# Performance work log

Measured on AMD Instinct MI355X. Metric: run time of the kernel, lower is better.

The kernel has to match this reference:

```python
import jax, jax.numpy as jnp
import numpy as np

B, H, S, D = 4, 16, 2048, 64
INV_SCALE_FACTOR = 8.0  # scores are divided by this (== sqrt(D))
DROPOUT_P = 0.0         # deterministic baseline; dropout is identity at p=0


def setup_inputs() -> dict:
    key = jax.random.key(0)
    kq, kk, kv = jax.random.split(key, 3)
    return {
        "query": jax.random.normal(kq, (B, H, S, D), dtype=jnp.float32),
        "key": jax.random.normal(kk, (B, H, S, D), dtype=jnp.float32),
        "value": jax.random.normal(kv, (B, H, S, D), dtype=jnp.float32),
    }


def reference(query, key, value):
    # scores: [B, H, Sq, Sk]
    scores = jnp.einsum("bhqd,bhkd->bhqk", query, key) / INV_SCALE_FACTOR
    probs = jax.nn.softmax(scores, axis=-1)
    # dropout_p == 0.0 -> identity
    out = jnp.einsum("bhqk,bhkd->bhqd", probs, value)
    return out
```

## Files before the change

kernel.cpp:

```cpp
#include <hip/hip_runtime.h>


#define S_LEN 2048
#define D_DIM 64
#define TK    64
#define NTILE (S_LEN / TK)
#define LOG2E_OVER8 0.18033688011112042f
#define VROW  72
#define VTILE (64 * VROW)
#define VBH   (NTILE * VTILE)

typedef __bf16 bf16x8 __attribute__((ext_vector_type(8)));
typedef __bf16 bf16x4 __attribute__((ext_vector_type(4)));
typedef short  s16x4  __attribute__((ext_vector_type(4)));
typedef float  f32x4  __attribute__((ext_vector_type(4)));
typedef unsigned short us;

__device__ __forceinline__ us f2bf(float f) {
    union { __bf16 h; us u; } c;
    c.h = (__bf16)f;
    return c.u;
}

__device__ __forceinline__ unsigned pk2(float a, float b) {
#if __has_builtin(__builtin_amdgcn_cvt_pk_bf16_f32)
    typedef __bf16 bf2 __attribute__((ext_vector_type(2)));
    union { bf2 h; unsigned u; } c;
    c.h = __builtin_amdgcn_cvt_pk_bf16_f32(a, b);
    return c.u;
#else
    return ((unsigned)f2bf(b) << 16) | f2bf(a);
#endif
}

__device__ __forceinline__ float fast_exp2(float x) {
#if __has_builtin(__builtin_amdgcn_exp2f)
    return __builtin_amdgcn_exp2f(x);
#else
    return exp2f(x);
#endif
}

__device__ __forceinline__ void gload_lds16(const void* g, void* l) {
    __builtin_amdgcn_global_load_lds(
        (const __attribute__((address_space(1))) unsigned int*)g,
        (__attribute__((address_space(3))) unsigned int*)l, 16, 0, 0);
}

__device__ __forceinline__ f32x4 mfma16x16x16(s16x4 a, s16x4 b, f32x4 c) {
#if __has_builtin(__builtin_amdgcn_mfma_f32_16x16x16bf16_1k)
    return __builtin_amdgcn_mfma_f32_16x16x16bf16_1k(a, b, c, 0, 0, 0);
#else
    f32x4 d = c;
    asm volatile("v_mfma_f32_16x16x16_bf16 %0, %1, %2, %0"
                 : "+v"(d) : "v"(a), "v"(b));
    return d;
#endif
}

__global__ __launch_bounds__(256)
void prep(const float* __restrict__ K, const float* __restrict__ V,
          us* __restrict__ Kb, us* __restrict__ Vt) {
    __shared__ us Ls[64 * 68];
    const int bx = blockIdx.x, tid = threadIdx.x;
    if (bx < 4096) {
        const size_t i = ((size_t)bx * 256 + tid) * 8;
        const float4 a = *(const float4*)(K + i);
        const float4 b = *(const float4*)(K + i + 4);
        union { us u[8]; uint4 q; } pk;
        pk.u[0] = f2bf(a.x); pk.u[1] = f2bf(a.y);
        pk.u[2] = f2bf(a.z); pk.u[3] = f2bf(a.w);
        pk.u[4] = f2bf(b.x); pk.u[5] = f2bf(b.y);
        pk.u[6] = f2bf(b.z); pk.u[7] = f2bf(b.w);
        *(uint4*)(Kb + i) = pk.q;
    } else {
        const int idx = bx - 4096;
        const int t = idx & (NTILE - 1), bh = idx >> 5;
        {
            const int r = tid >> 2, seg = tid & 3;
            const float* src = V + ((size_t)bh * S_LEN + t * TK + r) * D_DIM + seg * 16;
            us* dst = &Ls[r * 68 + seg * 16];
#pragma unroll
            for (int i = 0; i < 2; ++i) {
                const float4 v0 = *(const float4*)(src + 8 * i);
                const float4 v1 = *(const float4*)(src + 8 * i + 4);
                union { us u[8]; uint2 q[2]; } pk;
                pk.u[0] = f2bf(v0.x); pk.u[1] = f2bf(v0.y);
                pk.u[2] = f2bf(v0.z); pk.u[3] = f2bf(v0.w);
                pk.u[4] = f2bf(v1.x); pk.u[5] = f2bf(v1.y);
                pk.u[6] = f2bf(v1.z); pk.u[7] = f2bf(v1.w);
                *(uint2*)(dst + 8 * i) = pk.q[0];
                *(uint2*)(dst + 8 * i + 4) = pk.q[1];
            }
        }
        __syncthreads();
        {
            const int d = tid >> 2, sc = tid & 3;
            union { us u[16]; uint4 q[2]; } pk;
#pragma unroll
            for (int j = 0; j < 16; ++j) pk.u[j] = Ls[(sc * 16 + j) * 68 + d];
            us* dst = Vt + (size_t)bh * VBH + t * VTILE + d * VROW + sc * 16;
            *(uint4*)(dst) = pk.q[0];
            *(uint4*)(dst + 8) = pk.q[1];
        }
    }
}

__global__ __launch_bounds__(256, 4)
void fa_fwd(const float* __restrict__ Qg, const us* __restrict__ Kb,
            const us* __restrict__ Vtb, float* __restrict__ Og) {
    __shared__ __align__(16) us Kl[2][TK * 64];
    __shared__ __align__(16) us Vl[2][VTILE];

    const int tid  = threadIdx.x;
    const int w    = tid >> 6;
    const int lane = tid & 63;
    const int l15  = lane & 15;
    const int quad = lane >> 4;
    const int x    = l15 & 7;

    const int bid   = blockIdx.x;
    const int chunk = bid >> 3;
    const int bh    = ((bid & 7) << 3) | (chunk >> 4);
    const int qb    = chunk & 15;
    const size_t base = (size_t)bh * S_LEN * D_DIM;

    bf16x8 bq00, bq01, bq10, bq11;
    {
        const float* q0 = Qg + base + (size_t)(qb * 128 + w * 32 + l15) * D_DIM + quad * 8;
        const float* q1 = q0 + 16 * D_DIM;
#define LOADQ(dst0, dst1, p)                                                  \
        {                                                                     \
            const float4 x0 = *(const float4*)(p);                            \
            const float4 x1 = *(const float4*)((p) + 4);                      \
            const float4 y0 = *(const float4*)((p) + 32);                     \
            const float4 y1 = *(const float4*)((p) + 36);                     \
            dst0[0]=(__bf16)(x0.x*LOG2E_OVER8); dst0[1]=(__bf16)(x0.y*LOG2E_OVER8); \
            dst0[2]=(__bf16)(x0.z*LOG2E_OVER8); dst0[3]=(__bf16)(x0.w*LOG2E_OVER8); \
            dst0[4]=(__bf16)(x1.x*LOG2E_OVER8); dst0[5]=(__bf16)(x1.y*LOG2E_OVER8); \
            dst0[6]=(__bf16)(x1.z*LOG2E_OVER8); dst0[7]=(__bf16)(x1.w*LOG2E_OVER8); \
            dst1[0]=(__bf16)(y0.x*LOG2E_OVER8); dst1[1]=(__bf16)(y0.y*LOG2E_OVER8); \
            dst1[2]=(__bf16)(y0.z*LOG2E_OVER8); dst1[3]=(__bf16)(y0.w*LOG2E_OVER8); \
            dst1[4]=(__bf16)(y1.x*LOG2E_OVER8); dst1[5]=(__bf16)(y1.y*LOG2E_OVER8); \
            dst1[6]=(__bf16)(y1.z*LOG2E_OVER8); dst1[7]=(__bf16)(y1.w*LOG2E_OVER8); \
        }
        LOADQ(bq00, bq01, q0)
        LOADQ(bq10, bq11, q1)
#undef LOADQ
    }

    const int krow   = w * 16 + (lane >> 3);
    const int kchunk = (lane & 7) ^ (lane >> 3);
    const us* ksrc = Kb + base + (size_t)krow * D_DIM + kchunk * 8;
    const us* vsrc = Vtb + (size_t)bh * VBH + lane * 8;

    f32x4 lv0 = {0.f, 0.f, 0.f, 0.f}, lv1 = {0.f, 0.f, 0.f, 0.f};
    f32x4 oa0[4], oa1[4];
#pragma unroll
    for (int db = 0; db < 4; ++db) {
        oa0[db] = (f32x4){0.f, 0.f, 0.f, 0.f};
        oa1[db] = (f32x4){0.f, 0.f, 0.f, 0.f};
    }

#pragma unroll
    for (int j = 0; j < 2; ++j)
        gload_lds16(ksrc + j * 512, &Kl[0][w * 1024 + j * 512]);
#pragma unroll
    for (int j = 0; j < 2; ++j)
        gload_lds16(vsrc + (w * 2 + j) * 512, &Vl[0][(w * 2 + j) * 512]);
    if (w == 0) gload_lds16(vsrc + 8 * 512, &Vl[0][8 * 512]);
    __syncthreads();

#pragma unroll 1
    for (int t = 0; t < NTILE; ++t) {
        const int cur = t & 1;
        if (t + 1 < NTILE) {
            const us* ks = ksrc + (size_t)(t + 1) * (TK * D_DIM);
            const us* vs = vsrc + (size_t)(t + 1) * VTILE;
            us* kd = &Kl[cur ^ 1][w * 1024];
            us* vd = &Vl[cur ^ 1][0];
#pragma unroll
            for (int j = 0; j < 2; ++j)
                gload_lds16(ks + j * 512, kd + j * 512);
#pragma unroll
            for (int j = 0; j < 2; ++j)
                gload_lds16(vs + (w * 2 + j) * 512, vd + (w * 2 + j) * 512);
            if (w == 0) gload_lds16(vs + 8 * 512, vd + 8 * 512);
        }

        const us* kl = Kl[cur];
        const us* vl = Vl[cur];
#pragma unroll
        for (int kb = 0; kb < 4; ++kb) {
            const int row = kb * 16 + l15;
            const bf16x8 a0 = *(const bf16x8*)&kl[row * 64 + ((quad ^ x) * 8)];
            const bf16x8 a1 = *(const bf16x8*)&kl[row * 64 + (((4 + quad) ^ x) * 8)];
            f32x4 c0 = {0.f, 0.f, 0.f, 0.f};
            c0 = __builtin_amdgcn_mfma_f32_16x16x32_bf16(a0, bq00, c0, 0, 0, 0);
            c0 = __builtin_amdgcn_mfma_f32_16x16x32_bf16(a1, bq01, c0, 0, 0, 0);
            f32x4 c1 = {0.f, 0.f, 0.f, 0.f};
            c1 = __builtin_amdgcn_mfma_f32_16x16x32_bf16(a0, bq10, c1, 0, 0, 0);
            c1 = __builtin_amdgcn_mfma_f32_16x16x32_bf16(a1, bq11, c1, 0, 0, 0);

            const float p00 = fast_exp2(c0[0]);
            const float p01 = fast_exp2(c0[1]);
            const float p02 = fast_exp2(c0[2]);
            const float p03 = fast_exp2(c0[3]);
            lv0 += (f32x4){p00, p01, p02, p03};
            const float p10 = fast_exp2(c1[0]);
            const float p11 = fast_exp2(c1[1]);
            const float p12 = fast_exp2(c1[2]);
            const float p13 = fast_exp2(c1[3]);
            lv1 += (f32x4){p10, p11, p12, p13};
            union { unsigned u[2]; s16x4 s; } bu0, bu1;
            bu0.u[0] = pk2(p00, p01);
            bu0.u[1] = pk2(p02, p03);
            bu1.u[0] = pk2(p10, p11);
            bu1.u[1] = pk2(p12, p13);

#pragma unroll
            for (int db = 0; db < 4; ++db) {
                union { bf16x4 h; s16x4 s; } au;
                au.h = *(const bf16x4*)&vl[l15 * VROW + quad * 4 + db * (16 * VROW) + kb * 16];
                oa0[db] = mfma16x16x16(au.s, bu0.s, oa0[db]);
                oa1[db] = mfma16x16x16(au.s, bu1.s, oa1[db]);
            }
        }
        __syncthreads();
    }

    float lq0 = lv0[0] + lv0[1] + lv0[2] + lv0[3];
    lq0 += __shfl_xor(lq0, 16, 64);
    lq0 += __shfl_xor(lq0, 32, 64);
    float lq1 = lv1[0] + lv1[1] + lv1[2] + lv1[3];
    lq1 += __shfl_xor(lq1, 16, 64);
    lq1 += __shfl_xor(lq1, 32, 64);
    const float inv0 = 1.f / lq0;
    const float inv1 = 1.f / lq1;
    float* op0 = Og + base + (size_t)(qb * 128 + w * 32 + l15) * D_DIM + quad * 4;
    float* op1 = op0 + 16 * D_DIM;
#pragma unroll
    for (int db = 0; db < 4; ++db) {
        float4 v0 = { oa0[db][0] * inv0, oa0[db][1] * inv0,
                      oa0[db][2] * inv0, oa0[db][3] * inv0 };
        *(float4*)(op0 + db * 16) = v0;
        float4 v1 = { oa1[db][0] * inv1, oa1[db][1] * inv1,
                      oa1[db][2] * inv1, oa1[db][3] * inv1 };
        *(float4*)(op1 + db * 16) = v1;
    }
}

extern "C" void kernel_launch(void* const* d_in, const int* in_sizes, int n_in,
                              void* d_out, int out_size, void* d_ws, size_t ws_size,
                              hipStream_t stream) {
    const float* Q = (const float*)d_in[0];
    const float* K = (const float*)d_in[1];
    const float* V = (const float*)d_in[2];
    float* O = (float*)d_out;

    us* Kb = (us*)d_ws;
    us* Vt = Kb + (size_t)64 * S_LEN * D_DIM;

    prep<<<4096 + 2048, 256, 0, stream>>>(K, V, Kb, Vt);
    fa_fwd<<<dim3(1024), 256, 0, stream>>>(Q, Kb, Vt, O);
}
```

Before: 235.1 us.

## Load V tiles directly from global into registers in MFMA fragment layout

The preprocessing kernel now writes transposed V in the exact per-lane MFMA A-fragment order, so each lane can fetch its V operands with 16-byte global loads straight into registers. This removes the LDS staging buffer for V and its shared-memory reads, which frees LDS and may raise occupancy. The QK and PV stages are regrouped into pairs of k-blocks so the V global loads can be issued ahead of use. In exchange, V reads now go through global/L2 latency inside the loop with no LDS double buffering, which could stall if the latency is not hidden.

```diff
diff --git a/kernel.cpp b/kernel.cpp
--- a/kernel.cpp
+++ b/kernel.cpp
@@ -6,12 +6,10 @@
 #define TK    64
 #define NTILE (S_LEN / TK)
 #define LOG2E_OVER8 0.18033688011112042f
-#define VROW  72
-#define VTILE (64 * VROW)
+#define VTILE (64 * 64)
 #define VBH   (NTILE * VTILE)
 
 typedef __bf16 bf16x8 __attribute__((ext_vector_type(8)));
-typedef __bf16 bf16x4 __attribute__((ext_vector_type(4)));
 typedef short  s16x4  __attribute__((ext_vector_type(4)));
 typedef float  f32x4  __attribute__((ext_vector_type(4)));
 typedef unsigned short us;
@@ -95,13 +93,20 @@
         }
         __syncthreads();
         {
-            const int d = tid >> 2, sc = tid & 3;
-            union { us u[16]; uint4 q[2]; } pk;
-#pragma unroll
-            for (int j = 0; j < 16; ++j) pk.u[j] = Ls[(sc * 16 + j) * 68 + d];
-            us* dst = Vt + (size_t)bh * VBH + t * VTILE + d * VROW + sc * 16;
-            *(uint4*)(dst) = pk.q[0];
-            *(uint4*)(dst + 8) = pk.q[1];
+            const int lane = tid & 63, db = tid >> 6;
+            const int quad = lane >> 4, l15 = lane & 15;
+            const int d = db * 16 + l15;
+            us* dst = Vt + (size_t)bh * VBH + t * VTILE + lane * 8;
+#pragma unroll
+            for (int c = 0; c < 2; ++c) {
+                union { us u[8]; uint4 q; } pk;
+#pragma unroll
+                for (int e = 0; e < 8; ++e) {
+                    const int k = (2 * c + (e >> 2)) * 16 + quad * 4 + (e & 3);
+                    pk.u[e] = Ls[k * 68 + d];
+                }
+                *(uint4*)(dst + (c * 4 + db) * 512) = pk.q;
+            }
         }
     }
 }
@@ -110,7 +115,6 @@
 void fa_fwd(const float* __restrict__ Qg, const us* __restrict__ Kb,
             const us* __restrict__ Vtb, float* __restrict__ Og) {
     __shared__ __align__(16) us Kl[2][TK * 64];
-    __shared__ __align__(16) us Vl[2][VTILE];
 
     const int tid  = threadIdx.x;
     const int w    = tid >> 6;
@@ -152,9 +156,9 @@
     const int krow   = w * 16 + (lane >> 3);
     const int kchunk = (lane & 7) ^ (lane >> 3);
     const us* ksrc = Kb + base + (size_t)krow * D_DIM + kchunk * 8;
-    const us* vsrc = Vtb + (size_t)bh * VBH + lane * 8;
-
-    f32x4 lv0 = {0.f, 0.f, 0.f, 0.f}, lv1 = {0.f, 0.f, 0.f, 0.f};
+    const us* vg0 = Vtb + (size_t)bh * VBH + lane * 8;
+
+    float lv0 = 0.f, lv1 = 0.f;
     f32x4 oa0[4], oa1[4];
 #pragma unroll
     for (int db = 0; db < 4; ++db) {
@@ -165,74 +169,82 @@
 #pragma unroll
     for (int j = 0; j < 2; ++j)
         gload_lds16(ksrc + j * 512, &Kl[0][w * 1024 + j * 512]);
-#pragma unroll
-    for (int j = 0; j < 2; ++j)
-        gload_lds16(vsrc + (w * 2 + j) * 512, &Vl[0][(w * 2 + j) * 512]);
-    if (w == 0) gload_lds16(vsrc + 8 * 512, &Vl[0][8 * 512]);
     __syncthreads();
+
+    s16x4 bus0[4], bus1[4];
+
+#define QK_STEP(kb)                                                            \
+    {                                                                          \
+        const int row_ = (kb) * 16 + l15;                                      \
+        const bf16x8 a0 = *(const bf16x8*)&kl[row_ * 64 + ((quad ^ x) * 8)];   \
+        const bf16x8 a1 = *(const bf16x8*)&kl[row_ * 64 + (((4 + quad) ^ x) * 8)]; \
+        f32x4 c0 = {0.f, 0.f, 0.f, 0.f};                                       \
+        c0 = __builtin_amdgcn_mfma_f32_16x16x32_bf16(a0, bq00, c0, 0, 0, 0);   \
+        c0 = __builtin_amdgcn_mfma_f32_16x16x32_bf16(a1, bq01, c0, 0, 0, 0);   \
+        f32x4 c1 = {0.f, 0.f, 0.f, 0.f};                                       \
+        c1 = __builtin_amdgcn_mfma_f32_16x16x32_bf16(a0, bq10, c1, 0, 0, 0);   \
+        c1 = __builtin_amdgcn_mfma_f32_16x16x32_bf16(a1, bq11, c1, 0, 0, 0);   \
+        const float p00 = fast_exp2(c0[0]), p01 = fast_exp2(c0[1]);            \
+        const float p02 = fast_exp2(c0[2]), p03 = fast_exp2(c0[3]);            \
+        lv0 += (p00 + p01) + (p02 + p03);                                      \
+        const float p10 = fast_exp2(c1[0]), p11 = fast_exp2(c1[1]);            \
+        const float p12 = fast_exp2(c1[2]), p13 = fast_exp2(c1[3]);            \
+        lv1 += (p10 + p11) + (p12 + p13);                                      \
+        union { unsigned u[2]; s16x4 s; } b0_, b1_;                            \
+        b0_.u[0] = pk2(p00, p01); b0_.u[1] = pk2(p02, p03);                    \
+        b1_.u[0] = pk2(p10, p11); b1_.u[1] = pk2(p12, p13);                    \
+        bus0[kb] = b0_.s; bus1[kb] = b1_.s;                                    \
+    }
+
+#define PV_PAIR(K0)                                                            \
+    _Pragma("unroll")                                                          \
+    for (int db = 0; db < 4; ++db) {                                           \
+        union { uint4 q; s16x4 s[2]; } va;                                     \
+        va.q = vqa[db];                                                        \
+        oa0[db] = mfma16x16x16(va.s[0], bus0[K0], oa0[db]);                    \
+        oa1[db] = mfma16x16x16(va.s[0], bus1[K0], oa1[db]);                    \
+        oa0[db] = mfma16x16x16(va.s[1], bus0[(K0) + 1], oa0[db]);              \
+        oa1[db] = mfma16x16x16(va.s[1], bus1[(K0) + 1], oa1[db]);              \
+    }
 
 #pragma unroll 1
     for (int t = 0; t < NTILE; ++t) {
         const int cur = t & 1;
+        const us* kl = Kl[cur];
+        const us* vg = vg0 + (size_t)t * VTILE;
+
+        uint4 vqa[4];
+#pragma unroll
+        for (int f = 0; f < 4; ++f) vqa[f] = *(const uint4*)(vg + f * 512);
+
+        QK_STEP(0)
+        QK_STEP(1)
+        PV_PAIR(0)
+
+#pragma unroll
+        for (int f = 0; f < 4; ++f) vqa[f] = *(const uint4*)(vg + (4 + f) * 512);
+
         if (t + 1 < NTILE) {
             const us* ks = ksrc + (size_t)(t + 1) * (TK * D_DIM);
-            const us* vs = vsrc + (size_t)(t + 1) * VTILE;
             us* kd = &Kl[cur ^ 1][w * 1024];
-            us* vd = &Vl[cur ^ 1][0];
 #pragma unroll
             for (int j = 0; j < 2; ++j)
                 gload_lds16(ks + j * 512, kd + j * 512);
-#pragma unroll
-            for (int j = 0; j < 2; ++j)
-                gload_lds16(vs + (w * 2 + j) * 512, vd + (w * 2 + j) * 512);
-            if (w == 0) gload_lds16(vs + 8 * 512, vd + 8 * 512);
-        }
-
-        const us* kl = Kl[cur];
-        const us* vl = Vl[cur];
-#pragma unroll
-        for (int kb = 0; kb < 4; ++kb) {
-            const int row = kb * 16 + l15;
-            const bf16x8 a0 = *(const bf16x8*)&kl[row * 64 + ((quad ^ x) * 8)];
-            const bf16x8 a1 = *(const bf16x8*)&kl[row * 64 + (((4 + quad) ^ x) * 8)];
-            f32x4 c0 = {0.f, 0.f, 0.f, 0.f};
-            c0 = __builtin_amdgcn_mfma_f32_16x16x32_bf16(a0, bq00, c0, 0, 0, 0);
-            c0 = __builtin_amdgcn_mfma_f32_16x16x32_bf16(a1, bq01, c0, 0, 0, 0);
-            f32x4 c1 = {0.f, 0.f, 0.f, 0.f};
-            c1 = __builtin_amdgcn_mfma_f32_16x16x32_bf16(a0, bq10, c1, 0, 0, 0);
-            c1 = __builtin_amdgcn_mfma_f32_16x16x32_bf16(a1, bq11, c1, 0, 0, 0);
-
-            const float p00 = fast_exp2(c0[0]);
-            const float p01 = fast_exp2(c0[1]);
-            const float p02 = fast_exp2(c0[2]);
-            const float p03 = fast_exp2(c0[3]);
-            lv0 += (f32x4){p00, p01, p02, p03};
-            const float p10 = fast_exp2(c1[0]);
-            const float p11 = fast_exp2(c1[1]);
-            const float p12 = fast_exp2(c1[2]);
-            const float p13 = fast_exp2(c1[3]);
-            lv1 += (f32x4){p10, p11, p12, p13};
-            union { unsigned u[2]; s16x4 s; } bu0, bu1;
-            bu0.u[0] = pk2(p00, p01);
-            bu0.u[1] = pk2(p02, p03);
-            bu1.u[0] = pk2(p10, p11);
-            bu1.u[1] = pk2(p12, p13);
-
-#pragma unroll
-            for (int db = 0; db < 4; ++db) {
-                union { bf16x4 h; s16x4 s; } au;
-                au.h = *(const bf16x4*)&vl[l15 * VROW + quad * 4 + db * (16 * VROW) + kb * 16];
-                oa0[db] = mfma16x16x16(au.s, bu0.s, oa0[db]);
-                oa1[db] = mfma16x16x16(au.s, bu1.s, oa1[db]);
-            }
-        }
+        }
+
+        QK_STEP(2)
+        QK_STEP(3)
+        PV_PAIR(2)
+
         __syncthreads();
     }
-
-    float lq0 = lv0[0] + lv0[1] + lv0[2] + lv0[3];
+#undef QK_STEP
+#undef PV_PAIR
+
+    float lq0 = lv0;
     lq0 += __shfl_xor(lq0, 16, 64);
     lq0 += __shfl_xor(lq0, 32, 64);
-    float lq1 = lv1[0] + lv1[1] + lv1[2] + lv1[3];
+    float lq1 = lv1;
     lq1 += __shfl_xor(lq1, 16, 64);
     lq1 += __shfl_xor(lq1, 32, 64);
     const float inv0 = 1.f / lq0;
```

Result: faster. 212.6 us (-9.5%).
